# Kernel optimization log

Measured on AMD Instinct MI355X. Metric: run time of the kernel, lower is better.

The kernel has to match this reference:

```python
import jax, jax.numpy as jnp
import numpy as np

EPS = 1e-8


def _laplace_normalize(edge_row, edge_col, edge_vals, num_nodes):
    # D_r^{-1/2} A D_c^{-1/2} as in laplace_transform
    deg_r = jax.ops.segment_sum(edge_vals, edge_row, num_segments=num_nodes)
    deg_c = jax.ops.segment_sum(edge_vals, edge_col, num_segments=num_nodes)
    inv_r = 1.0 / (jnp.sqrt(deg_r) + EPS)
    inv_c = 1.0 / (jnp.sqrt(deg_c) + EPS)
    return edge_vals * inv_r[edge_row] * inv_c[edge_col]


def _l2norm(x):
    # F.normalize(p=2, dim=1): x / max(||x||, eps) with eps=1e-12
    n = jnp.sqrt(jnp.sum(x * x, axis=1, keepdims=True))
    return x / jnp.maximum(n, 1e-12)


def setup_inputs() -> dict:
    key = jax.random.key(0)
    k1, k2, k3, k4, k5, k6 = jax.random.split(key, 6)
    N, D, E, B = 100000, 64, 3200000, 4096
    node_features = jax.random.normal(k1, (N, D), dtype=jnp.float32)
    edge_row = jax.random.randint(k2, (E,), 0, N, dtype=jnp.int32)
    edge_col = jax.random.randint(k3, (E,), 0, N, dtype=jnp.int32)
    edge_vals = jnp.ones((E,), dtype=jnp.float32)
    a_id = jax.random.randint(k4, (B,), 0, N, dtype=jnp.int32)
    pos_id = jax.random.randint(k5, (B,), 0, N, dtype=jnp.int32)
    neg_id = jax.random.randint(k6, (B,), 0, N, dtype=jnp.int32)
    return {"node_features": node_features, "edge_row": edge_row,
            "edge_col": edge_col, "edge_vals": edge_vals,
            "a_id": a_id, "pos_id": pos_id, "neg_id": neg_id}


def reference(node_features, edge_row, edge_col, edge_vals, a_id, pos_id, neg_id):
    num_nodes = node_features.shape[0]
    num_layers = 3
    norm_vals = _laplace_normalize(edge_row, edge_col, edge_vals, num_nodes)

    # one_propagate: repeated spmm + per-layer L2 normalize, mean over layers
    features = node_features
    acc = node_features  # layer-0 term of the running sum (not normalized)
    for _ in range(num_layers):
        msgs = norm_vals[:, None] * features[edge_col]  # [E, D]
        features = jax.ops.segment_sum(msgs, edge_row, num_segments=num_nodes)
        acc = acc + _l2norm(features)
    node_rep = acc / (num_layers + 1)

    # BPR loss over batch
    a = node_rep[a_id]
    pos_pred = jnp.sum(a * node_rep[pos_id], axis=1)
    neg_pred = jnp.sum(a * node_rep[neg_id], axis=1)
    loss = jnp.mean(-jax.nn.log_sigmoid(pos_pred - neg_pred))
    return loss
```

## Files before the change

kernel.cpp:

```cpp
#include <hip/hip_runtime.h>
#include <math.h>

#define DDIM 64
#define BUCKET 1024
#define LRSHIFT 17
#define CMASK 0x1FFFF
#define LRMASK 0x3FF
#define NBLK 512
#define TPB_BIN 1024
#define NWV 16
#define TPB_CP 512
#define MAXNB 128

typedef unsigned long long ull;
typedef _Float16 half2_t __attribute__((ext_vector_type(2)));

__device__ inline unsigned int bf16_hi(float v) {
    unsigned int a = __float_as_uint(v);
    return (a + 0x7fffu + ((a >> 16) & 1u)) & 0xffff0000u;
}

__device__ inline unsigned int pk_f16x2(float lo, float hi) {
    return __builtin_bit_cast(unsigned int, __builtin_amdgcn_cvt_pkrtz(lo, hi));
}

__device__ inline half2_t dup_lo16(unsigned int s) {
    return __builtin_bit_cast(half2_t, __builtin_amdgcn_perm(0u, s, 0x01000100u));
}

__device__ inline half2_t h2_shfl_xor(half2_t v, int off) {
    return __builtin_bit_cast(half2_t, __shfl_xor(__builtin_bit_cast(unsigned int, v), off));
}

__global__ void init_fill_kernel(int* __restrict__ gfill_r, int* __restrict__ gfill_c,
                                 int NB, int cap) {
    int k = blockIdx.x * blockDim.x + threadIdx.x;
    if (k < NB) {
        gfill_r[k * 16] = k * cap;
        gfill_c[k * 16] = k * cap;
    }
}

__global__ __launch_bounds__(TPB_BIN)
void binning_kernel(const int* __restrict__ erow, const int* __restrict__ ecol,
                    const float* __restrict__ evals,
                    int* __restrict__ gfill_r, int* __restrict__ gfill_c,
                    ull* __restrict__ br, unsigned int* __restrict__ bc,
                    int E, int NB, int chunk) {
    __shared__ int hr[NWV][MAXNB];
    __shared__ int hc[NWV][MAXNB];
    __shared__ int fr[MAXNB];
    __shared__ int fc[MAXNB];
    int t = threadIdx.x;
    int wv = t >> 6;
    for (int k = t; k < NWV * MAXNB; k += TPB_BIN) { (&hr[0][0])[k] = 0; (&hc[0][0])[k] = 0; }
    __syncthreads();
    int lo = blockIdx.x * chunk;
    int hi = min(E, lo + chunk);
    int nq = (hi - lo) >> 2;
    int rem = (hi - lo) & 3;
    int p0 = t, p1 = t + TPB_BIN;
    bool h0 = p0 < nq, h1 = p1 < nq;
    int4 r40, c40, r41, c41;
    float4 v40, v41;
    if (h0) {
        int i = lo + 4 * p0;
        r40 = *(const int4*)(erow + i);
        c40 = *(const int4*)(ecol + i);
        v40 = *(const float4*)(evals + i);
        atomicAdd(&hr[wv][r40.x >> 10], 1);
        atomicAdd(&hr[wv][r40.y >> 10], 1);
        atomicAdd(&hr[wv][r40.z >> 10], 1);
        atomicAdd(&hr[wv][r40.w >> 10], 1);
        atomicAdd(&hc[wv][c40.x >> 10], 1);
        atomicAdd(&hc[wv][c40.y >> 10], 1);
        atomicAdd(&hc[wv][c40.z >> 10], 1);
        atomicAdd(&hc[wv][c40.w >> 10], 1);
    }
    if (h1) {
        int i = lo + 4 * p1;
        r41 = *(const int4*)(erow + i);
        c41 = *(const int4*)(ecol + i);
        v41 = *(const float4*)(evals + i);
        atomicAdd(&hr[wv][r41.x >> 10], 1);
        atomicAdd(&hr[wv][r41.y >> 10], 1);
        atomicAdd(&hr[wv][r41.z >> 10], 1);
        atomicAdd(&hr[wv][r41.w >> 10], 1);
        atomicAdd(&hc[wv][c41.x >> 10], 1);
        atomicAdd(&hc[wv][c41.y >> 10], 1);
        atomicAdd(&hc[wv][c41.z >> 10], 1);
        atomicAdd(&hc[wv][c41.w >> 10], 1);
    }
    if (t == 0) {
        for (int i = hi - rem; i < hi; i++) {
            atomicAdd(&hr[0][erow[i] >> 10], 1);
            atomicAdd(&hc[0][ecol[i] >> 10], 1);
        }
    }
    __syncthreads();
    if (t < NB) {
        int sr = 0, sc = 0;
        #pragma unroll
        for (int w2 = 0; w2 < NWV; w2++) { sr += hr[w2][t]; sc += hc[w2][t]; }
        fr[t] = atomicAdd(&gfill_r[t * 16], sr);
        fc[t] = atomicAdd(&gfill_c[t * 16], sc);
    }
    __syncthreads();
    if (h0) {
        int pos0 = atomicAdd(&fr[r40.x >> 10], 1);
        int pos1 = atomicAdd(&fr[r40.y >> 10], 1);
        int pos2 = atomicAdd(&fr[r40.z >> 10], 1);
        int pos3 = atomicAdd(&fr[r40.w >> 10], 1);
        br[pos0] = ((ull)__float_as_uint(v40.x) << 32) | ((ull)(r40.x & 1023) << LRSHIFT) | (unsigned)c40.x;
        br[pos1] = ((ull)__float_as_uint(v40.y) << 32) | ((ull)(r40.y & 1023) << LRSHIFT) | (unsigned)c40.y;
        br[pos2] = ((ull)__float_as_uint(v40.z) << 32) | ((ull)(r40.z & 1023) << LRSHIFT) | (unsigned)c40.z;
        br[pos3] = ((ull)__float_as_uint(v40.w) << 32) | ((ull)(r40.w & 1023) << LRSHIFT) | (unsigned)c40.w;
        int q0 = atomicAdd(&fc[c40.x >> 10], 1);
        int q1 = atomicAdd(&fc[c40.y >> 10], 1);
        int q2 = atomicAdd(&fc[c40.z >> 10], 1);
        int q3 = atomicAdd(&fc[c40.w >> 10], 1);
        bc[q0] = bf16_hi(v40.x) | (unsigned)(c40.x & 1023);
        bc[q1] = bf16_hi(v40.y) | (unsigned)(c40.y & 1023);
        bc[q2] = bf16_hi(v40.z) | (unsigned)(c40.z & 1023);
        bc[q3] = bf16_hi(v40.w) | (unsigned)(c40.w & 1023);
    }
    if (h1) {
        int pos0 = atomicAdd(&fr[r41.x >> 10], 1);
        int pos1 = atomicAdd(&fr[r41.y >> 10], 1);
        int pos2 = atomicAdd(&fr[r41.z >> 10], 1);
        int pos3 = atomicAdd(&fr[r41.w >> 10], 1);
        br[pos0] = ((ull)__float_as_uint(v41.x) << 32) | ((ull)(r41.x & 1023) << LRSHIFT) | (unsigned)c41.x;
        br[pos1] = ((ull)__float_as_uint(v41.y) << 32) | ((ull)(r41.y & 1023) << LRSHIFT) | (unsigned)c41.y;
        br[pos2] = ((ull)__float_as_uint(v41.z) << 32) | ((ull)(r41.z & 1023) << LRSHIFT) | (unsigned)c41.z;
        br[pos3] = ((ull)__float_as_uint(v41.w) << 32) | ((ull)(r41.w & 1023) << LRSHIFT) | (unsigned)c41.w;
        int q0 = atomicAdd(&fc[c41.x >> 10], 1);
        int q1 = atomicAdd(&fc[c41.y >> 10], 1);
        int q2 = atomicAdd(&fc[c41.z >> 10], 1);
        int q3 = atomicAdd(&fc[c41.w >> 10], 1);
        bc[q0] = bf16_hi(v41.x) | (unsigned)(c41.x & 1023);
        bc[q1] = bf16_hi(v41.y) | (unsigned)(c41.y & 1023);
        bc[q2] = bf16_hi(v41.z) | (unsigned)(c41.z & 1023);
        bc[q3] = bf16_hi(v41.w) | (unsigned)(c41.w & 1023);
    }
    if (t == 0) {
        for (int i = hi - rem; i < hi; i++) {
            int r = erow[i], c = ecol[i];
            float v = evals[i];
            int pos = atomicAdd(&fr[r >> 10], 1);
            br[pos] = ((ull)__float_as_uint(v) << 32) | ((ull)(r & 1023) << LRSHIFT) | (unsigned)c;
            int pos2 = atomicAdd(&fc[c >> 10], 1);
            bc[pos2] = bf16_hi(v) | (unsigned)(c & 1023);
        }
    }
}

__global__ __launch_bounds__(TPB_CP)
void count_kernel(const ull* __restrict__ br, const unsigned int* __restrict__ bc,
                  const int* __restrict__ gfill_r, const int* __restrict__ gfill_c,
                  int* __restrict__ subcnt, float* __restrict__ subds,
                  float* __restrict__ subdsc, int cap) {
    __shared__ int cnt[BUCKET];
    __shared__ float ds[BUCKET];
    __shared__ float dsc[BUCKET];
    int b = blockIdx.x >> 3, ch = blockIdx.x & 7;
    int t = threadIdx.x;
    for (int k = t; k < BUCKET; k += TPB_CP) { cnt[k] = 0; ds[k] = 0.0f; dsc[k] = 0.0f; }
    __syncthreads();
    int s = b * cap;
    int e = gfill_r[b * 16];
    int len = ((((e - s) + 7) >> 3) + 3) & ~3;
    int cs = s + ch * len, ce = min(e, cs + len);
    int m = cs + ((ce - cs) & ~3);
    for (int i = cs + 4 * t; i < m; i += 4 * TPB_CP) {
        ull p0 = br[i];
        ull p1 = br[i + 1];
        ull p2 = br[i + 2];
        ull p3 = br[i + 3];
        int lr0 = (int)((p0 >> LRSHIFT) & LRMASK);
        int lr1 = (int)((p1 >> LRSHIFT) & LRMASK);
        int lr2 = (int)((p2 >> LRSHIFT) & LRMASK);
        int lr3 = (int)((p3 >> LRSHIFT) & LRMASK);
        atomicAdd(&cnt[lr0], 1);
        atomicAdd(&cnt[lr1], 1);
        atomicAdd(&cnt[lr2], 1);
        atomicAdd(&cnt[lr3], 1);
        atomicAdd(&ds[lr0], __uint_as_float((unsigned)(p0 >> 32)));
        atomicAdd(&ds[lr1], __uint_as_float((unsigned)(p1 >> 32)));
        atomicAdd(&ds[lr2], __uint_as_float((unsigned)(p2 >> 32)));
        atomicAdd(&ds[lr3], __uint_as_float((unsigned)(p3 >> 32)));
    }
    if (t == 0) {
        for (int i = m; i < ce; i++) {
            ull p = br[i];
            int lr = (int)((p >> LRSHIFT) & LRMASK);
            atomicAdd(&cnt[lr], 1);
            atomicAdd(&ds[lr], __uint_as_float((unsigned)(p >> 32)));
        }
    }
    int e2 = gfill_c[b * 16];
    int len2 = ((((e2 - s) + 7) >> 3) + 3) & ~3;
    int cs2 = s + ch * len2, ce2 = min(e2, cs2 + len2);
    int m2 = cs2 + ((ce2 - cs2) & ~3);
    for (int i = cs2 + 4 * t; i < m2; i += 4 * TPB_CP) {
        uint4 p = *(const uint4*)(bc + i);
        atomicAdd(&dsc[p.x & 0x3FFu], __uint_as_float(p.x & 0xffff0000u));
        atomicAdd(&dsc[p.y & 0x3FFu], __uint_as_float(p.y & 0xffff0000u));
        atomicAdd(&dsc[p.z & 0x3FFu], __uint_as_float(p.z & 0xffff0000u));
        atomicAdd(&dsc[p.w & 0x3FFu], __uint_as_float(p.w & 0xffff0000u));
    }
    if (t == 0) {
        for (int i = m2; i < ce2; i++) {
            unsigned int p = bc[i];
            atomicAdd(&dsc[p & 0x3FFu], __uint_as_float(p & 0xffff0000u));
        }
    }
    __syncthreads();
    size_t base = ((size_t)b * 8 + ch) * BUCKET;
    for (int k = t; k < BUCKET; k += TPB_CP) {
        subcnt[base + k] = cnt[k];
        subds[base + k]  = ds[k];
        subdsc[base + k] = dsc[k];
    }
}

__global__ __launch_bounds__(1024)
void combine_kernel(int* __restrict__ subcnt, const float* __restrict__ subds,
                    const float* __restrict__ subdsc,
                    int2* __restrict__ rse,
                    float* __restrict__ inv_r, float* __restrict__ inv_c,
                    int N, int cap) {
    __shared__ int tot[BUCKET];
    int b = blockIdx.x, t = threadIdx.x;
    size_t base = (size_t)b * 8 * BUCKET;
    int c8[8];
    int sum = 0;
    #pragma unroll
    for (int c = 0; c < 8; c++) { c8[c] = subcnt[base + c * BUCKET + t]; sum += c8[c]; }
    int sum2 = (sum + 3) & ~3;
    tot[t] = sum2;
    __syncthreads();
    for (int off = 1; off < BUCKET; off <<= 1) {
        int v = (t >= off) ? tot[t - off] : 0;
        __syncthreads();
        tot[t] += v;
        __syncthreads();
    }
    int excl = tot[t] - sum2;
    int node = b * BUCKET + t;
    int s = b * cap;
    if (node < N) {
        int2 se;
        se.x = s + excl;
        se.y = s + excl + sum;
        rse[node] = se;
    }
    int run = s + excl;
    #pragma unroll
    for (int c = 0; c < 8; c++) { int v = c8[c]; subcnt[base + c * BUCKET + t] = run; run += v; }
    float d = 0.0f, dc = 0.0f;
    #pragma unroll
    for (int c = 0; c < 8; c++) { d += subds[base + c * BUCKET + t]; dc += subdsc[base + c * BUCKET + t]; }
    inv_r[b * BUCKET + t] = 1.0f / (sqrtf(d) + 1e-8f);
    inv_c[b * BUCKET + t] = 1.0f / (sqrtf(dc) + 1e-8f);
}

__global__ __launch_bounds__(TPB_CP)
void place_kernel(const ull* __restrict__ br, const int* __restrict__ gfill_r,
                  const int* __restrict__ pbase, const float* __restrict__ inv_r,
                  const float* __restrict__ inv_c,
                  unsigned int* __restrict__ cw, int cap) {
    __shared__ int fill[BUCKET];
    __shared__ float irs[BUCKET];
    int b = blockIdx.x >> 3, ch = blockIdx.x & 7;
    int t = threadIdx.x;
    size_t pb = ((size_t)b * 8 + ch) * BUCKET;
    for (int k = t; k < BUCKET; k += TPB_CP) {
        fill[k] = pbase[pb + k];
        irs[k]  = inv_r[b * BUCKET + k];
    }
    __syncthreads();
    int s = b * cap;
    int e = gfill_r[b * 16];
    int len = ((((e - s) + 7) >> 3) + 3) & ~3;
    int cs = s + ch * len, ce = min(e, cs + len);
    int m = cs + ((ce - cs) & ~3);
    for (int i = cs + 4 * t; i < m; i += 4 * TPB_CP) {
        ull p0 = br[i];
        ull p1 = br[i + 1];
        ull p2 = br[i + 2];
        ull p3 = br[i + 3];
        int c0 = (int)(p0 & CMASK), c1 = (int)(p1 & CMASK);
        int c2 = (int)(p2 & CMASK), c3 = (int)(p3 & CMASK);
        int lr0 = (int)((p0 >> LRSHIFT) & LRMASK);
        int lr1 = (int)((p1 >> LRSHIFT) & LRMASK);
        int lr2 = (int)((p2 >> LRSHIFT) & LRMASK);
        int lr3 = (int)((p3 >> LRSHIFT) & LRMASK);
        float v0 = __uint_as_float((unsigned)(p0 >> 32));
        float v1 = __uint_as_float((unsigned)(p1 >> 32));
        float v2 = __uint_as_float((unsigned)(p2 >> 32));
        float v3 = __uint_as_float((unsigned)(p3 >> 32));
        int pos0 = atomicAdd(&fill[lr0], 1);
        int pos1 = atomicAdd(&fill[lr1], 1);
        int pos2 = atomicAdd(&fill[lr2], 1);
        int pos3 = atomicAdd(&fill[lr3], 1);
        float w0 = v0 * inv_c[c0] * irs[lr0];
        float w1 = v1 * inv_c[c1] * irs[lr1];
        float w2 = v2 * inv_c[c2] * irs[lr2];
        float w3 = v3 * inv_c[c3] * irs[lr3];
        cw[pos0] = ((unsigned)c0 << 15) | ((pk_f16x2(w0, w0) & 0xFFFFu) >> 1);
        cw[pos1] = ((unsigned)c1 << 15) | ((pk_f16x2(w1, w1) & 0xFFFFu) >> 1);
        cw[pos2] = ((unsigned)c2 << 15) | ((pk_f16x2(w2, w2) & 0xFFFFu) >> 1);
        cw[pos3] = ((unsigned)c3 << 15) | ((pk_f16x2(w3, w3) & 0xFFFFu) >> 1);
    }
    if (t == 0) {
        for (int i = m; i < ce; i++) {
            ull p = br[i];
            int c = (int)(p & CMASK);
            int lr = (int)((p >> LRSHIFT) & LRMASK);
            float v = __uint_as_float((unsigned)(p >> 32));
            int pos = atomicAdd(&fill[lr], 1);
            float wv = v * inv_c[c] * irs[lr];
            cw[pos] = ((unsigned)c << 15) | ((pk_f16x2(wv, wv) & 0xFFFFu) >> 1);
        }
    }
}

__global__ void cvt_kernel(const float* __restrict__ src,
                           unsigned int* __restrict__ dst, long n4) {
    long i = (long)blockIdx.x * blockDim.x + threadIdx.x;
    if (i < n4) {
        float4 v = ((const float4*)src)[i];
        uint2 o;
        o.x = pk_f16x2(v.x, v.y);
        o.y = pk_f16x2(v.z, v.w);
        ((uint2*)dst)[i] = o;
    }
}

__global__ __launch_bounds__(256)
void spmm_f16_kernel(const int2* __restrict__ rse,
                     const unsigned int* __restrict__ cw,
                     const unsigned short* __restrict__ fin,
                     unsigned short* __restrict__ fout, int N) {
    int wid = blockIdx.x * (blockDim.x >> 6) + (threadIdx.x >> 6);
    if (wid >= N) return;
    int lane = threadIdx.x & 63;
    int g = lane >> 3;
    int h = lane & 7;
    int2 se = rse[wid];
    int s = se.x, e = se.y;
    half2_t a2[8];
    #pragma unroll
    for (int k = 0; k < 8; k++) a2[k] = (half2_t)0;

    for (int base = s; base < e; base += 32) {
        int j = base + 4 * g;
        if (j < e) {
            uint4 pw = *(const uint4*)(cw + j);
            int c0 = (int)(pw.x >> 15);
            int c1 = (j + 1 < e) ? (int)(pw.y >> 15) : c0;
            int c2 = (j + 2 < e) ? (int)(pw.z >> 15) : c0;
            int c3 = (j + 3 < e) ? (int)(pw.w >> 15) : c0;
            uint4 q0 = ((const uint4*)(fin + ((long)c0 << 6)))[h];
            uint4 q1 = ((const uint4*)(fin + ((long)c1 << 6)))[h];
            uint4 q2 = ((const uint4*)(fin + ((long)c2 << 6)))[h];
            uint4 q3 = ((const uint4*)(fin + ((long)c3 << 6)))[h];
            half2_t w0 = dup_lo16(pw.x << 1);
            half2_t w1 = (j + 1 < e) ? dup_lo16(pw.y << 1) : (half2_t)0;
            half2_t w2 = (j + 2 < e) ? dup_lo16(pw.z << 1) : (half2_t)0;
            half2_t w3 = (j + 3 < e) ? dup_lo16(pw.w << 1) : (half2_t)0;
            a2[0] += w0 * __builtin_bit_cast(half2_t, q0.x);
            a2[1] += w0 * __builtin_bit_cast(half2_t, q0.y);
            a2[2] += w0 * __builtin_bit_cast(half2_t, q0.z);
            a2[3] += w0 * __builtin_bit_cast(half2_t, q0.w);
            a2[4] += w1 * __builtin_bit_cast(half2_t, q1.x);
            a2[5] += w1 * __builtin_bit_cast(half2_t, q1.y);
            a2[6] += w1 * __builtin_bit_cast(half2_t, q1.z);
            a2[7] += w1 * __builtin_bit_cast(half2_t, q1.w);
            a2[0] += w2 * __builtin_bit_cast(half2_t, q2.x);
            a2[1] += w2 * __builtin_bit_cast(half2_t, q2.y);
            a2[2] += w2 * __builtin_bit_cast(half2_t, q2.z);
            a2[3] += w2 * __builtin_bit_cast(half2_t, q2.w);
            a2[4] += w3 * __builtin_bit_cast(half2_t, q3.x);
            a2[5] += w3 * __builtin_bit_cast(half2_t, q3.y);
            a2[6] += w3 * __builtin_bit_cast(half2_t, q3.z);
            a2[7] += w3 * __builtin_bit_cast(half2_t, q3.w);
        }
    }

    #pragma unroll
    for (int k = 0; k < 4; k++) a2[k] += a2[k + 4];
    #pragma unroll
    for (int k = 0; k < 4; k++) {
        a2[k] += h2_shfl_xor(a2[k], 8);
        a2[k] += h2_shfl_xor(a2[k], 16);
        a2[k] += h2_shfl_xor(a2[k], 32);
    }
    if (g == 0) {
        uint4 o;
        o.x = __builtin_bit_cast(unsigned int, a2[0]);
        o.y = __builtin_bit_cast(unsigned int, a2[1]);
        o.z = __builtin_bit_cast(unsigned int, a2[2]);
        o.w = __builtin_bit_cast(unsigned int, a2[3]);
        ((uint4*)(fout + ((long)wid << 6)))[h] = o;
    }
}

__device__ inline float rep_at(const float* __restrict__ nf,
                               const unsigned short* __restrict__ f1,
                               const unsigned short* __restrict__ f2,
                               const unsigned short* __restrict__ f3,
                               int id, int lane) {
    long off = (long)id * DDIM + lane;
    float r  = nf[off];
    float v1 = (float)__builtin_bit_cast(_Float16, f1[off]);
    float v2 = (float)__builtin_bit_cast(_Float16, f2[off]);
    float v3 = (float)__builtin_bit_cast(_Float16, f3[off]);
    float s1 = v1 * v1, s2 = v2 * v2, s3 = v3 * v3;
    #pragma unroll
    for (int o = 1; o < 64; o <<= 1) {
        s1 += __shfl_xor(s1, o);
        s2 += __shfl_xor(s2, o);
        s3 += __shfl_xor(s3, o);
    }
    r += v1 / fmaxf(sqrtf(s1), 1e-12f);
    r += v2 / fmaxf(sqrtf(s2), 1e-12f);
    r += v3 / fmaxf(sqrtf(s3), 1e-12f);
    return r;
}

__global__ void loss_terms_kernel(const float* __restrict__ nf,
                                  const unsigned short* __restrict__ f1,
                                  const unsigned short* __restrict__ f2,
                                  const unsigned short* __restrict__ f3,
                                  const int* __restrict__ a_id, const int* __restrict__ p_id,
                                  const int* __restrict__ n_id,
                                  float* __restrict__ terms, int B) {
    long gid = (long)blockIdx.x * blockDim.x + threadIdx.x;
    int b = (int)(gid >> 6);
    int lane = threadIdx.x & 63;
    if (b < B) {
        float ra = rep_at(nf, f1, f2, f3, a_id[b], lane);
        float rp = rep_at(nf, f1, f2, f3, p_id[b], lane);
        float rn = rep_at(nf, f1, f2, f3, n_id[b], lane);
        float dp = ra * rp, dn = ra * rn;
        #pragma unroll
        for (int off = 1; off < 64; off <<= 1) { dp += __shfl_xor(dp, off); dn += __shfl_xor(dn, off); }
        if (lane == 0) {
            float x = (dp - dn) * 0.0625f;
            terms[b] = fmaxf(-x, 0.0f) + log1pf(expf(-fabsf(x)));
        }
    }
}

__global__ void reduce_kernel(const float* __restrict__ terms, float* __restrict__ out, int B) {
    __shared__ float sm[256];
    float s = 0.0f;
    for (int i = threadIdx.x; i < B; i += 256) s += terms[i];
    sm[threadIdx.x] = s;
    __syncthreads();
    for (int stride = 128; stride > 0; stride >>= 1) {
        if (threadIdx.x < stride) sm[threadIdx.x] += sm[threadIdx.x + stride];
        __syncthreads();
    }
    if (threadIdx.x == 0) out[0] = sm[0] / (float)B;
}

extern "C" void kernel_launch(void* const* d_in, const int* in_sizes, int n_in,
                              void* d_out, int out_size, void* d_ws, size_t ws_size,
                              hipStream_t stream) {
    const float* nf    = (const float*)d_in[0];
    const int*   erow  = (const int*)d_in[1];
    const int*   ecol  = (const int*)d_in[2];
    const float* evals = (const float*)d_in[3];
    const int*   a_id  = (const int*)d_in[4];
    const int*   p_id  = (const int*)d_in[5];
    const int*   n_id  = (const int*)d_in[6];

    int N = in_sizes[0] / DDIM;
    int E = in_sizes[1];
    int B = in_sizes[4];
    int NB = (N + BUCKET - 1) / BUCKET;
    int chunk = (((E + NBLK - 1) / NBLK) + 3) & ~3;
    int Npad = NB * BUCKET;

    long capl = ((long)E * BUCKET) / N;
    int cap = (int)(capl + capl / 12 + 5120);
    cap = (cap + 63) & ~63;

    size_t regionA = (size_t)cap * NB * 8;
    size_t regionB = (size_t)cap * NB * 4;
    size_t featB16 = (size_t)N * DDIM * 2;
    if (regionA < 2 * featB16) regionA = 2 * featB16;
    size_t subBytes = (size_t)NB * 8 * BUCKET * 4;

    char* w = (char*)d_ws;
    ull*  br     = (ull*)w;
    char* regAp  = w;                 w += regionA;
    unsigned int* bc = (unsigned int*)w;
    unsigned int* cw = (unsigned int*)w;  w += regionB + 256;
    unsigned short* fb2 = (unsigned short*)w;  w += featB16;
    int* subcnt  = (int*)w;           w += subBytes;
    float* subds = (float*)w;         w += subBytes;
    float* subdsc= (float*)w;         w += subBytes;
    float* inv_c = (float*)w;         w += (size_t)Npad * 4;
    float* inv_r = (float*)w;         w += (size_t)Npad * 4;
    int2* rse    = (int2*)w;          w += (size_t)N * 8;
    int* gfill_r = (int*)w;           w += (size_t)NB * 16 * 4;
    int* gfill_c = (int*)w;           w += (size_t)NB * 16 * 4;
    float* terms = (float*)w;         w += (size_t)B * 4;

    unsigned short* fb0 = (unsigned short*)regAp;
    unsigned short* fb1 = (unsigned short*)(regAp + featB16);

    init_fill_kernel<<<1, 128, 0, stream>>>(gfill_r, gfill_c, NB, cap);
    binning_kernel<<<NBLK, TPB_BIN, 0, stream>>>(erow, ecol, evals, gfill_r, gfill_c,
                                                 br, bc, E, NB, chunk);
    count_kernel<<<NB * 8, TPB_CP, 0, stream>>>(br, bc, gfill_r, gfill_c,
                                                subcnt, subds, subdsc, cap);
    combine_kernel<<<NB, 1024, 0, stream>>>(subcnt, subds, subdsc, rse,
                                            inv_r, inv_c, N, cap);
    place_kernel<<<NB * 8, TPB_CP, 0, stream>>>(br, gfill_r, subcnt, inv_r, inv_c, cw, cap);

    long n4 = (long)N * DDIM / 4;
    cvt_kernel<<<(unsigned)((n4 + 255) / 256), 256, 0, stream>>>(nf, (unsigned int*)fb0, n4);

    unsigned spmmGrid = (unsigned)((N + 3) / 4);
    spmm_f16_kernel<<<spmmGrid, 256, 0, stream>>>(rse, cw, fb0, fb1, N);
    spmm_f16_kernel<<<spmmGrid, 256, 0, stream>>>(rse, cw, fb1, fb2, N);
    spmm_f16_kernel<<<spmmGrid, 256, 0, stream>>>(rse, cw, fb2, fb0, N);

    loss_terms_kernel<<<(unsigned)(((long)B * 64 + 255) / 256), 256, 0, stream>>>(
        nf, fb1, fb2, fb0, a_id, p_id, n_id, terms, B);
    reduce_kernel<<<1, 256, 0, stream>>>(terms, (float*)d_out, B);
}
```

Baseline: 382.5 us.

## Fuse count/combine/place into one per-bucket kernel and fold column scaling into features

Bucket size drops from 1024 to 256 nodes, so one 256-thread block can own a whole bucket. The separate count, combine and place kernels become a single kernel that counts, scans, computes inverse degrees and places the edges, removing the sub-count buffers and two launches. The per-edge inv_c gather is dropped from edge weights. Instead inv_c is applied to the features: it scales the input during fp16 conversion and each spmm output row, and the per-layer L2 normalise cancels that scale in the loss. The trade-off is far more buckets with fewer blocks per bucket, a changed capacity formula, and extra fp16 rounding from the feature scaling.

Result: faster. 367.5 us (-3.9%).

```diff
diff --git a/kernel.cpp b/kernel.cpp
--- a/kernel.cpp
+++ b/kernel.cpp
@@ -2,15 +2,14 @@
 #include <math.h>
 
 #define DDIM 64
-#define BUCKET 1024
+#define BUCKET 256
 #define LRSHIFT 17
 #define CMASK 0x1FFFF
-#define LRMASK 0x3FF
+#define LRMASK 0xFF
 #define NBLK 512
 #define TPB_BIN 1024
 #define NWV 16
-#define TPB_CP 512
-#define MAXNB 128
+#define MAXNB 400
 
 typedef unsigned long long ull;
 typedef _Float16 half2_t __attribute__((ext_vector_type(2)));
@@ -68,33 +67,33 @@
         r40 = *(const int4*)(erow + i);
         c40 = *(const int4*)(ecol + i);
         v40 = *(const float4*)(evals + i);
-        atomicAdd(&hr[wv][r40.x >> 10], 1);
-        atomicAdd(&hr[wv][r40.y >> 10], 1);
-        atomicAdd(&hr[wv][r40.z >> 10], 1);
-        atomicAdd(&hr[wv][r40.w >> 10], 1);
-        atomicAdd(&hc[wv][c40.x >> 10], 1);
-        atomicAdd(&hc[wv][c40.y >> 10], 1);
-        atomicAdd(&hc[wv][c40.z >> 10], 1);
-        atomicAdd(&hc[wv][c40.w >> 10], 1);
+        atomicAdd(&hr[wv][r40.x >> 8], 1);
+        atomicAdd(&hr[wv][r40.y >> 8], 1);
+        atomicAdd(&hr[wv][r40.z >> 8], 1);
+        atomicAdd(&hr[wv][r40.w >> 8], 1);
+        atomicAdd(&hc[wv][c40.x >> 8], 1);
+        atomicAdd(&hc[wv][c40.y >> 8], 1);
+        atomicAdd(&hc[wv][c40.z >> 8], 1);
+        atomicAdd(&hc[wv][c40.w >> 8], 1);
     }
     if (h1) {
         int i = lo + 4 * p1;
         r41 = *(const int4*)(erow + i);
         c41 = *(const int4*)(ecol + i);
         v41 = *(const float4*)(evals + i);
-        atomicAdd(&hr[wv][r41.x >> 10], 1);
-        atomicAdd(&hr[wv][r41.y >> 10], 1);
-        atomicAdd(&hr[wv][r41.z >> 10], 1);
-        atomicAdd(&hr[wv][r41.w >> 10], 1);
-        atomicAdd(&hc[wv][c41.x >> 10], 1);
-        atomicAdd(&hc[wv][c41.y >> 10], 1);
-        atomicAdd(&hc[wv][c41.z >> 10], 1);
-        atomicAdd(&hc[wv][c41.w >> 10], 1);
+        atomicAdd(&hr[wv][r41.x >> 8], 1);
+        atomicAdd(&hr[wv][r41.y >> 8], 1);
+        atomicAdd(&hr[wv][r41.z >> 8], 1);
+        atomicAdd(&hr[wv][r41.w >> 8], 1);
+        atomicAdd(&hc[wv][c41.x >> 8], 1);
+        atomicAdd(&hc[wv][c41.y >> 8], 1);
+        atomicAdd(&hc[wv][c41.z >> 8], 1);
+        atomicAdd(&hc[wv][c41.w >> 8], 1);
     }
     if (t == 0) {
         for (int i = hi - rem; i < hi; i++) {
-            atomicAdd(&hr[0][erow[i] >> 10], 1);
-            atomicAdd(&hc[0][ecol[i] >> 10], 1);
+            atomicAdd(&hr[0][erow[i] >> 8], 1);
+            atomicAdd(&hc[0][ecol[i] >> 8], 1);
         }
     }
     __syncthreads();
@@ -107,71 +106,70 @@
     }
     __syncthreads();
     if (h0) {
-        int pos0 = atomicAdd(&fr[r40.x >> 10], 1);
-        int pos1 = atomicAdd(&fr[r40.y >> 10], 1);
-        int pos2 = atomicAdd(&fr[r40.z >> 10], 1);
-        int pos3 = atomicAdd(&fr[r40.w >> 10], 1);
-        br[pos0] = ((ull)__float_as_uint(v40.x) << 32) | ((ull)(r40.x & 1023) << LRSHIFT) | (unsigned)c40.x;
-        br[pos1] = ((ull)__float_as_uint(v40.y) << 32) | ((ull)(r40.y & 1023) << LRSHIFT) | (unsigned)c40.y;
-        br[pos2] = ((ull)__float_as_uint(v40.z) << 32) | ((ull)(r40.z & 1023) << LRSHIFT) | (unsigned)c40.z;
-        br[pos3] = ((ull)__float_as_uint(v40.w) << 32) | ((ull)(r40.w & 1023) << LRSHIFT) | (unsigned)c40.w;
-        int q0 = atomicAdd(&fc[c40.x >> 10], 1);
-        int q1 = atomicAdd(&fc[c40.y >> 10], 1);
-        int q2 = atomicAdd(&fc[c40.z >> 10], 1);
-        int q3 = atomicAdd(&fc[c40.w >> 10], 1);
-        bc[q0] = bf16_hi(v40.x) | (unsigned)(c40.x & 1023);
-        bc[q1] = bf16_hi(v40.y) | (unsigned)(c40.y & 1023);
-        bc[q2] = bf16_hi(v40.z) | (unsigned)(c40.z & 1023);
-        bc[q3] = bf16_hi(v40.w) | (unsigned)(c40.w & 1023);
+        int pos0 = atomicAdd(&fr[r40.x >> 8], 1);
+        int pos1 = atomicAdd(&fr[r40.y >> 8], 1);
+        int pos2 = atomicAdd(&fr[r40.z >> 8], 1);
+        int pos3 = atomicAdd(&fr[r40.w >> 8], 1);
+        br[pos0] = ((ull)__float_as_uint(v40.x) << 32) | ((ull)(r40.x & 255) << LRSHIFT) | (unsigned)c40.x;
+        br[pos1] = ((ull)__float_as_uint(v40.y) << 32) | ((ull)(r40.y & 255) << LRSHIFT) | (unsigned)c40.y;
+        br[pos2] = ((ull)__float_as_uint(v40.z) << 32) | ((ull)(r40.z & 255) << LRSHIFT) | (unsigned)c40.z;
+        br[pos3] = ((ull)__float_as_uint(v40.w) << 32) | ((ull)(r40.w & 255) << LRSHIFT) | (unsigned)c40.w;
+        int q0 = atomicAdd(&fc[c40.x >> 8], 1);
+        int q1 = atomicAdd(&fc[c40.y >> 8], 1);
+        int q2 = atomicAdd(&fc[c40.z >> 8], 1);
+        int q3 = atomicAdd(&fc[c40.w >> 8], 1);
+        bc[q0] = bf16_hi(v40.x) | (unsigned)(c40.x & 255);
+        bc[q1] = bf16_hi(v40.y) | (unsigned)(c40.y & 255);
+        bc[q2] = bf16_hi(v40.z) | (unsigned)(c40.z & 255);
+        bc[q3] = bf16_hi(v40.w) | (unsigned)(c40.w & 255);
     }
     if (h1) {
-        int pos0 = atomicAdd(&fr[r41.x >> 10], 1);
-        int pos1 = atomicAdd(&fr[r41.y >> 10], 1);
-        int pos2 = atomicAdd(&fr[r41.z >> 10], 1);
-        int pos3 = atomicAdd(&fr[r41.w >> 10], 1);
-        br[pos0] = ((ull)__float_as_uint(v41.x) << 32) | ((ull)(r41.x & 1023) << LRSHIFT) | (unsigned)c41.x;
-        br[pos1] = ((ull)__float_as_uint(v41.y) << 32) | ((ull)(r41.y & 1023) << LRSHIFT) | (unsigned)c41.y;
-        br[pos2] = ((ull)__float_as_uint(v41.z) << 32) | ((ull)(r41.z & 1023) << LRSHIFT) | (unsigned)c41.z;
-        br[pos3] = ((ull)__float_as_uint(v41.w) << 32) | ((ull)(r41.w & 1023) << LRSHIFT) | (unsigned)c41.w;
-        int q0 = atomicAdd(&fc[c41.x >> 10], 1);
-        int q1 = atomicAdd(&fc[c41.y >> 10], 1);
-        int q2 = atomicAdd(&fc[c41.z >> 10], 1);
-        int q3 = atomicAdd(&fc[c41.w >> 10], 1);
-        bc[q0] = bf16_hi(v41.x) | (unsigned)(c41.x & 1023);
-        bc[q1] = bf16_hi(v41.y) | (unsigned)(c41.y & 1023);
-        bc[q2] = bf16_hi(v41.z) | (unsigned)(c41.z & 1023);
-        bc[q3] = bf16_hi(v41.w) | (unsigned)(c41.w & 1023);
+        int pos0 = atomicAdd(&fr[r41.x >> 8], 1);
+        int pos1 = atomicAdd(&fr[r41.y >> 8], 1);
+        int pos2 = atomicAdd(&fr[r41.z >> 8], 1);
+        int pos3 = atomicAdd(&fr[r41.w >> 8], 1);
+        br[pos0] = ((ull)__float_as_uint(v41.x) << 32) | ((ull)(r41.x & 255) << LRSHIFT) | (unsigned)c41.x;
+        br[pos1] = ((ull)__float_as_uint(v41.y) << 32) | ((ull)(r41.y & 255) << LRSHIFT) | (unsigned)c41.y;
+        br[pos2] = ((ull)__float_as_uint(v41.z) << 32) | ((ull)(r41.z & 255) << LRSHIFT) | (unsigned)c41.z;
+        br[pos3] = ((ull)__float_as_uint(v41.w) << 32) | ((ull)(r41.w & 255) << LRSHIFT) | (unsigned)c41.w;
+        int q0 = atomicAdd(&fc[c41.x >> 8], 1);
+        int q1 = atomicAdd(&fc[c41.y >> 8], 1);
+        int q2 = atomicAdd(&fc[c41.z >> 8], 1);
+        int q3 = atomicAdd(&fc[c41.w >> 8], 1);
+        bc[q0] = bf16_hi(v41.x) | (unsigned)(c41.x & 255);
+        bc[q1] = bf16_hi(v41.y) | (unsigned)(c41.y & 255);
+        bc[q2] = bf16_hi(v41.z) | (unsigned)(c41.z & 255);
+        bc[q3] = bf16_hi(v41.w) | (unsigned)(c41.w & 255);
     }
     if (t == 0) {
         for (int i = hi - rem; i < hi; i++) {
             int r = erow[i], c = ecol[i];
             float v = evals[i];
-            int pos = atomicAdd(&fr[r >> 10], 1);
-            br[pos] = ((ull)__float_as_uint(v) << 32) | ((ull)(r & 1023) << LRSHIFT) | (unsigned)c;
-            int pos2 = atomicAdd(&fc[c >> 10], 1);
-            bc[pos2] = bf16_hi(v) | (unsigned)(c & 1023);
-        }
-    }
-}
-
-__global__ __launch_bounds__(TPB_CP)
-void count_kernel(const ull* __restrict__ br, const unsigned int* __restrict__ bc,
-                  const int* __restrict__ gfill_r, const int* __restrict__ gfill_c,
-                  int* __restrict__ subcnt, float* __restrict__ subds,
-                  float* __restrict__ subdsc, int cap) {
-    __shared__ int cnt[BUCKET];
+            int pos = atomicAdd(&fr[r >> 8], 1);
+            br[pos] = ((ull)__float_as_uint(v) << 32) | ((ull)(r & 255) << LRSHIFT) | (unsigned)c;
+            int pos2 = atomicAdd(&fc[c >> 8], 1);
+            bc[pos2] = bf16_hi(v) | (unsigned)(c & 255);
+        }
+    }
+}
+
+__global__ __launch_bounds__(BUCKET)
+void fused_cp_kernel(const ull* __restrict__ br, const unsigned int* __restrict__ bc,
+                     const int* __restrict__ gfill_r, const int* __restrict__ gfill_c,
+                     int2* __restrict__ rse, float* __restrict__ inv_c,
+                     unsigned int* __restrict__ cw, int N, int cap) {
+    __shared__ int   cnt[BUCKET];
     __shared__ float ds[BUCKET];
     __shared__ float dsc[BUCKET];
-    int b = blockIdx.x >> 3, ch = blockIdx.x & 7;
-    int t = threadIdx.x;
-    for (int k = t; k < BUCKET; k += TPB_CP) { cnt[k] = 0; ds[k] = 0.0f; dsc[k] = 0.0f; }
+    __shared__ int   sc[BUCKET];
+    __shared__ float invr[BUCKET];
+    int b = blockIdx.x, t = threadIdx.x;
+    cnt[t] = 0; ds[t] = 0.0f; dsc[t] = 0.0f;
     __syncthreads();
     int s = b * cap;
     int e = gfill_r[b * 16];
-    int len = ((((e - s) + 7) >> 3) + 3) & ~3;
-    int cs = s + ch * len, ce = min(e, cs + len);
-    int m = cs + ((ce - cs) & ~3);
-    for (int i = cs + 4 * t; i < m; i += 4 * TPB_CP) {
+    int m = s + ((e - s) & ~3);
+    for (int i = s + 4 * t; i < m; i += 4 * BUCKET) {
         ull p0 = br[i];
         ull p1 = br[i + 1];
         ull p2 = br[i + 2];
@@ -190,7 +188,7 @@
         atomicAdd(&ds[lr3], __uint_as_float((unsigned)(p3 >> 32)));
     }
     if (t == 0) {
-        for (int i = m; i < ce; i++) {
+        for (int i = m; i < e; i++) {
             ull p = br[i];
             int lr = (int)((p >> LRSHIFT) & LRMASK);
             atomicAdd(&cnt[lr], 1);
@@ -198,99 +196,50 @@
         }
     }
     int e2 = gfill_c[b * 16];
-    int len2 = ((((e2 - s) + 7) >> 3) + 3) & ~3;
-    int cs2 = s + ch * len2, ce2 = min(e2, cs2 + len2);
-    int m2 = cs2 + ((ce2 - cs2) & ~3);
-    for (int i = cs2 + 4 * t; i < m2; i += 4 * TPB_CP) {
+    int m2 = s + ((e2 - s) & ~3);
+    for (int i = s + 4 * t; i < m2; i += 4 * BUCKET) {
         uint4 p = *(const uint4*)(bc + i);
-        atomicAdd(&dsc[p.x & 0x3FFu], __uint_as_float(p.x & 0xffff0000u));
-        atomicAdd(&dsc[p.y & 0x3FFu], __uint_as_float(p.y & 0xffff0000u));
-        atomicAdd(&dsc[p.z & 0x3FFu], __uint_as_float(p.z & 0xffff0000u));
-        atomicAdd(&dsc[p.w & 0x3FFu], __uint_as_float(p.w & 0xffff0000u));
+        atomicAdd(&dsc[p.x & 0xFFu], __uint_as_float(p.x & 0xffff0000u));
+        atomicAdd(&dsc[p.y & 0xFFu], __uint_as_float(p.y & 0xffff0000u));
+        atomicAdd(&dsc[p.z & 0xFFu], __uint_as_float(p.z & 0xffff0000u));
+        atomicAdd(&dsc[p.w & 0xFFu], __uint_as_float(p.w & 0xffff0000u));
     }
     if (t == 0) {
-        for (int i = m2; i < ce2; i++) {
+        for (int i = m2; i < e2; i++) {
             unsigned int p = bc[i];
-            atomicAdd(&dsc[p & 0x3FFu], __uint_as_float(p & 0xffff0000u));
-        }
-    }
-    __syncthreads();
-    size_t base = ((size_t)b * 8 + ch) * BUCKET;
-    for (int k = t; k < BUCKET; k += TPB_CP) {
-        subcnt[base + k] = cnt[k];
-        subds[base + k]  = ds[k];
-        subdsc[base + k] = dsc[k];
-    }
-}
-
-__global__ __launch_bounds__(1024)
-void combine_kernel(int* __restrict__ subcnt, const float* __restrict__ subds,
-                    const float* __restrict__ subdsc,
-                    int2* __restrict__ rse,
-                    float* __restrict__ inv_r, float* __restrict__ inv_c,
-                    int N, int cap) {
-    __shared__ int tot[BUCKET];
-    int b = blockIdx.x, t = threadIdx.x;
-    size_t base = (size_t)b * 8 * BUCKET;
-    int c8[8];
-    int sum = 0;
-    #pragma unroll
-    for (int c = 0; c < 8; c++) { c8[c] = subcnt[base + c * BUCKET + t]; sum += c8[c]; }
-    int sum2 = (sum + 3) & ~3;
-    tot[t] = sum2;
+            atomicAdd(&dsc[p & 0xFFu], __uint_as_float(p & 0xffff0000u));
+        }
+    }
+    __syncthreads();
+    int c0 = cnt[t];
+    int sum4 = (c0 + 3) & ~3;
+    sc[t] = sum4;
     __syncthreads();
     for (int off = 1; off < BUCKET; off <<= 1) {
-        int v = (t >= off) ? tot[t - off] : 0;
+        int v = (t >= off) ? sc[t - off] : 0;
         __syncthreads();
-        tot[t] += v;
+        sc[t] += v;
         __syncthreads();
     }
-    int excl = tot[t] - sum2;
+    int st = s + sc[t] - sum4;
     int node = b * BUCKET + t;
-    int s = b * cap;
     if (node < N) {
         int2 se;
-        se.x = s + excl;
-        se.y = s + excl + sum;
+        se.x = st;
+        se.y = st + c0;
         rse[node] = se;
     }
-    int run = s + excl;
-    #pragma unroll
-    for (int c = 0; c < 8; c++) { int v = c8[c]; subcnt[base + c * BUCKET + t] = run; run += v; }
-    float d = 0.0f, dc = 0.0f;
-    #pragma unroll
-    for (int c = 0; c < 8; c++) { d += subds[base + c * BUCKET + t]; dc += subdsc[base + c * BUCKET + t]; }
-    inv_r[b * BUCKET + t] = 1.0f / (sqrtf(d) + 1e-8f);
-    inv_c[b * BUCKET + t] = 1.0f / (sqrtf(dc) + 1e-8f);
-}
-
-__global__ __launch_bounds__(TPB_CP)
-void place_kernel(const ull* __restrict__ br, const int* __restrict__ gfill_r,
-                  const int* __restrict__ pbase, const float* __restrict__ inv_r,
-                  const float* __restrict__ inv_c,
-                  unsigned int* __restrict__ cw, int cap) {
-    __shared__ int fill[BUCKET];
-    __shared__ float irs[BUCKET];
-    int b = blockIdx.x >> 3, ch = blockIdx.x & 7;
-    int t = threadIdx.x;
-    size_t pb = ((size_t)b * 8 + ch) * BUCKET;
-    for (int k = t; k < BUCKET; k += TPB_CP) {
-        fill[k] = pbase[pb + k];
-        irs[k]  = inv_r[b * BUCKET + k];
-    }
-    __syncthreads();
-    int s = b * cap;
-    int e = gfill_r[b * 16];
-    int len = ((((e - s) + 7) >> 3) + 3) & ~3;
-    int cs = s + ch * len, ce = min(e, cs + len);
-    int m = cs + ((ce - cs) & ~3);
-    for (int i = cs + 4 * t; i < m; i += 4 * TPB_CP) {
+    inv_c[node] = 1.0f / (sqrtf(dsc[t]) + 1e-8f);
+    invr[t] = 1.0f / (sqrtf(ds[t]) + 1e-8f);
+    cnt[t] = st;
+    __syncthreads();
+    for (int i = s + 4 * t; i < m; i += 4 * BUCKET) {
         ull p0 = br[i];
         ull p1 = br[i + 1];
         ull p2 = br[i + 2];
         ull p3 = br[i + 3];
-        int c0 = (int)(p0 & CMASK), c1 = (int)(p1 & CMASK);
-        int c2 = (int)(p2 & CMASK), c3 = (int)(p3 & CMASK);
+        int c0_ = (int)(p0 & CMASK), c1_ = (int)(p1 & CMASK);
+        int c2_ = (int)(p2 & CMASK), c3_ = (int)(p3 & CMASK);
         int lr0 = (int)((p0 >> LRSHIFT) & LRMASK);
         int lr1 = (int)((p1 >> LRSHIFT) & LRMASK);
         int lr2 = (int)((p2 >> LRSHIFT) & LRMASK);
@@ -299,40 +248,41 @@
         float v1 = __uint_as_float((unsigned)(p1 >> 32));
         float v2 = __uint_as_float((unsigned)(p2 >> 32));
         float v3 = __uint_as_float((unsigned)(p3 >> 32));
-        int pos0 = atomicAdd(&fill[lr0], 1);
-        int pos1 = atomicAdd(&fill[lr1], 1);
-        int pos2 = atomicAdd(&fill[lr2], 1);
-        int pos3 = atomicAdd(&fill[lr3], 1);
-        float w0 = v0 * inv_c[c0] * irs[lr0];
-        float w1 = v1 * inv_c[c1] * irs[lr1];
-        float w2 = v2 * inv_c[c2] * irs[lr2];
-        float w3 = v3 * inv_c[c3] * irs[lr3];
-        cw[pos0] = ((unsigned)c0 << 15) | ((pk_f16x2(w0, w0) & 0xFFFFu) >> 1);
-        cw[pos1] = ((unsigned)c1 << 15) | ((pk_f16x2(w1, w1) & 0xFFFFu) >> 1);
-        cw[pos2] = ((unsigned)c2 << 15) | ((pk_f16x2(w2, w2) & 0xFFFFu) >> 1);
-        cw[pos3] = ((unsigned)c3 << 15) | ((pk_f16x2(w3, w3) & 0xFFFFu) >> 1);
+        int pos0 = atomicAdd(&cnt[lr0], 1);
+        int pos1 = atomicAdd(&cnt[lr1], 1);
+        int pos2 = atomicAdd(&cnt[lr2], 1);
+        int pos3 = atomicAdd(&cnt[lr3], 1);
+        float w0 = v0 * invr[lr0];
+        float w1 = v1 * invr[lr1];
+        float w2 = v2 * invr[lr2];
+        float w3 = v3 * invr[lr3];
+        cw[pos0] = ((unsigned)c0_ << 15) | ((pk_f16x2(w0, w0) & 0xFFFFu) >> 1);
+        cw[pos1] = ((unsigned)c1_ << 15) | ((pk_f16x2(w1, w1) & 0xFFFFu) >> 1);
+        cw[pos2] = ((unsigned)c2_ << 15) | ((pk_f16x2(w2, w2) & 0xFFFFu) >> 1);
+        cw[pos3] = ((unsigned)c3_ << 15) | ((pk_f16x2(w3, w3) & 0xFFFFu) >> 1);
     }
     if (t == 0) {
-        for (int i = m; i < ce; i++) {
+        for (int i = m; i < e; i++) {
             ull p = br[i];
             int c = (int)(p & CMASK);
             int lr = (int)((p >> LRSHIFT) & LRMASK);
             float v = __uint_as_float((unsigned)(p >> 32));
-            int pos = atomicAdd(&fill[lr], 1);
-            float wv = v * inv_c[c] * irs[lr];
+            int pos = atomicAdd(&cnt[lr], 1);
+            float wv = v * invr[lr];
             cw[pos] = ((unsigned)c << 15) | ((pk_f16x2(wv, wv) & 0xFFFFu) >> 1);
         }
     }
 }
 
-__global__ void cvt_kernel(const float* __restrict__ src,
+__global__ void cvt_kernel(const float* __restrict__ src, const float* __restrict__ inv_c,
                            unsigned int* __restrict__ dst, long n4) {
     long i = (long)blockIdx.x * blockDim.x + threadIdx.x;
     if (i < n4) {
+        float ic = inv_c[i >> 4];
         float4 v = ((const float4*)src)[i];
         uint2 o;
-        o.x = pk_f16x2(v.x, v.y);
-        o.y = pk_f16x2(v.z, v.w);
+        o.x = pk_f16x2(v.x * ic, v.y * ic);
+        o.y = pk_f16x2(v.z * ic, v.w * ic);
         ((uint2*)dst)[i] = o;
     }
 }
@@ -340,6 +290,7 @@
 __global__ __launch_bounds__(256)
 void spmm_f16_kernel(const int2* __restrict__ rse,
                      const unsigned int* __restrict__ cw,
+                     const float* __restrict__ inv_c,
                      const unsigned short* __restrict__ fin,
                      unsigned short* __restrict__ fout, int N) {
     int wid = blockIdx.x * (blockDim.x >> 6) + (threadIdx.x >> 6);
@@ -348,6 +299,7 @@
     int g = lane >> 3;
     int h = lane & 7;
     int2 se = rse[wid];
+    float ic = inv_c[wid];
     int s = se.x, e = se.y;
     half2_t a2[8];
     #pragma unroll
@@ -397,11 +349,12 @@
         a2[k] += h2_shfl_xor(a2[k], 32);
     }
     if (g == 0) {
+        half2_t ich = __builtin_bit_cast(half2_t, pk_f16x2(ic, ic));
         uint4 o;
-        o.x = __builtin_bit_cast(unsigned int, a2[0]);
-        o.y = __builtin_bit_cast(unsigned int, a2[1]);
-        o.z = __builtin_bit_cast(unsigned int, a2[2]);
-        o.w = __builtin_bit_cast(unsigned int, a2[3]);
+        o.x = __builtin_bit_cast(unsigned int, a2[0] * ich);
+        o.y = __builtin_bit_cast(unsigned int, a2[1] * ich);
+        o.z = __builtin_bit_cast(unsigned int, a2[2] * ich);
+        o.w = __builtin_bit_cast(unsigned int, a2[3] * ich);
         ((uint4*)(fout + ((long)wid << 6)))[h] = o;
     }
 }
@@ -485,14 +438,13 @@
     int Npad = NB * BUCKET;
 
     long capl = ((long)E * BUCKET) / N;
-    int cap = (int)(capl + capl / 12 + 5120);
+    int cap = (int)(capl + capl / 8 + 2048);
     cap = (cap + 63) & ~63;
 
     size_t regionA = (size_t)cap * NB * 8;
     size_t regionB = (size_t)cap * NB * 4;
     size_t featB16 = (size_t)N * DDIM * 2;
     if (regionA < 2 * featB16) regionA = 2 * featB16;
-    size_t subBytes = (size_t)NB * 8 * BUCKET * 4;
 
     char* w = (char*)d_ws;
     ull*  br     = (ull*)w;
@@ -500,11 +452,7 @@
     unsigned int* bc = (unsigned int*)w;
     unsigned int* cw = (unsigned int*)w;  w += regionB + 256;
     unsigned short* fb2 = (unsigned short*)w;  w += featB16;
-    int* subcnt  = (int*)w;           w += subBytes;
-    float* subds = (float*)w;         w += subBytes;
-    float* subdsc= (float*)w;         w += subBytes;
     float* inv_c = (float*)w;         w += (size_t)Npad * 4;
-    float* inv_r = (float*)w;         w += (size_t)Npad * 4;
     int2* rse    = (int2*)w;          w += (size_t)N * 8;
     int* gfill_r = (int*)w;           w += (size_t)NB * 16 * 4;
     int* gfill_c = (int*)w;           w += (size_t)NB * 16 * 4;
@@ -513,22 +461,19 @@
     unsigned short* fb0 = (unsigned short*)regAp;
     unsigned short* fb1 = (unsigned short*)(regAp + featB16);
 
-    init_fill_kernel<<<1, 128, 0, stream>>>(gfill_r, gfill_c, NB, cap);
+    init_fill_kernel<<<(unsigned)((NB + 127) / 128), 128, 0, stream>>>(gfill_r, gfill_c, NB, cap);
     binning_kernel<<<NBLK, TPB_BIN, 0, stream>>>(erow, ecol, evals, gfill_r, gfill_c,
                                                  br, bc, E, NB, chunk);
-    count_kernel<<<NB * 8, TPB_CP, 0, stream>>>(br, bc, gfill_r, gfill_c,
-                                                subcnt, subds, subdsc, cap);
-    combine_kernel<<<NB, 1024, 0, stream>>>(subcnt, subds, subdsc, rse,
-                                            inv_r, inv_c, N, cap);
-    place_kernel<<<NB * 8, TPB_CP, 0, stream>>>(br, gfill_r, subcnt, inv_r, inv_c, cw, cap);
+    fused_cp_kernel<<<NB, BUCKET, 0, stream>>>(br, bc, gfill_r, gfill_c,
+                                               rse, inv_c, cw, N, cap);
 
     long n4 = (long)N * DDIM / 4;
-    cvt_kernel<<<(unsigned)((n4 + 255) / 256), 256, 0, stream>>>(nf, (unsigned int*)fb0, n4);
+    cvt_kernel<<<(unsigned)((n4 + 255) / 256), 256, 0, stream>>>(nf, inv_c, (unsigned int*)fb0, n4);
 
     unsigned spmmGrid = (unsigned)((N + 3) / 4);
-    spmm_f16_kernel<<<spmmGrid, 256, 0, stream>>>(rse, cw, fb0, fb1, N);
-    spmm_f16_kernel<<<spmmGrid, 256, 0, stream>>>(rse, cw, fb1, fb2, N);
-    spmm_f16_kernel<<<spmmGrid, 256, 0, stream>>>(rse, cw, fb2, fb0, N);
+    spmm_f16_kernel<<<spmmGrid, 256, 0, stream>>>(rse, cw, inv_c, fb0, fb1, N);
+    spmm_f16_kernel<<<spmmGrid, 256, 0, stream>>>(rse, cw, inv_c, fb1, fb2, N);
+    spmm_f16_kernel<<<spmmGrid, 256, 0, stream>>>(rse, cw, inv_c, fb2, fb0, N);
 
     loss_terms_kernel<<<(unsigned)(((long)B * 64 + 255) / 256), 256, 0, stream>>>(
         nf, fb1, fb2, fb0, a_id, p_id, n_id, terms, B);
```
